# Performance work log

Hardware: AMD Instinct MI355X
Metric: run time of the kernel (lower is better)

## Reference

```python
import jax, jax.numpy as jnp
import numpy as np

C_IN = 64      # in_channels
C_OUT = 64     # out_channels
LOC = 2        # locality_size
K = 2 * LOC + 1   # kernel size = 5
B, H, W = 4, 128, 128


def _init_lateral_weights():
    # Matches LateralLayer._init_lateral_weights: 1 at (co, co*K*K + LOC*K + LOC)
    w = np.zeros((C_OUT, C_IN * K * K), np.float32)
    for co in range(C_OUT):
        cii = co * K * K + LOC * K + LOC  # center tap of matching input channel
        w[co, cii] = 1.0
    return jnp.asarray(w).reshape(C_OUT, C_IN * K * K, 1, 1)


def setup_inputs() -> dict:
    key = jax.random.key(0)
    # binary input (the layer asserts x in {0,1})
    x = jax.random.bernoulli(key, 0.1, (B, C_IN, H, W)).astype(jnp.float32)
    return {"x": x, "W_lateral": _init_lateral_weights()}


def _rearrange(x):
    # Faithful to F.conv2d(x, W_rearrange, padding='same') with the one-hot
    # indicator kernel: out[b, i*K*K + j*K + kk, h, w] = x_pad[b, i, h+j, w+kk].
    # Implemented as an unfold via K*K shifted slices (same math, no O((CKK)^2) conv).
    p = LOC
    xp = jnp.pad(x, ((0, 0), (0, 0), (p, p), (p, p)))
    Hh, Ww = x.shape[2], x.shape[3]
    patches = [xp[:, :, j:j + Hh, kk:kk + Ww] for j in range(K) for kk in range(K)]
    xr = jnp.stack(patches, axis=2)              # (B, C, K*K, H, W)
    return xr.reshape(x.shape[0], x.shape[1] * K * K, Hh, Ww)


def reference(x, W_lateral):
    xr = _rearrange(x)                                  # (B, C*K*K, H, W)
    w = W_lateral.reshape(W_lateral.shape[0], -1)       # (O, C*K*K)
    # 1x1 conv == channel contraction
    x_lateral = jnp.einsum('bkhw,ok->bohw', xr, w)      # (B, O, H, W)
    # conv with ones_like(W_lateral) == channel sum, same for every out channel
    x_max_act = jnp.sum(xr, axis=1, keepdims=True)      # (B, 1, H, W)
    min_support = float(K)
    x_max_act = jnp.maximum(x_max_act, min_support)
    xn = x_lateral / x_max_act
    xn = xn / (1e-10 + jnp.sum(w, axis=1)[None, :, None, None])
    xn = xn / (1e-10 + jnp.max(xn, axis=(2, 3), keepdims=True))
    # ts == 0 -> no temporal averaging with x_lateral_norm_prev
    x_lateral_bin = (xn ** 3 >= 0.5).astype(jnp.float32)
    return x_lateral, xn, x_lateral_bin
```

## Files before the change

kernel.cpp:

```cpp
#include <hip/hip_runtime.h>

constexpr int Bb  = 4;
constexpr int C   = 64;
constexpr int H   = 128;
constexpr int Wd  = 128;
constexpr int K   = 5;
constexpr int LOC = 2;
constexpr int KK  = K * K;
constexpr int CKK = C * KK;
constexpr int HW  = H * Wd;
constexpr int N   = Bb * C * HW;

typedef float v4f __attribute__((ext_vector_type(4)));

__device__ __forceinline__ float frcp(float x) { return __builtin_amdgcn_rcpf(x); }
__device__ __forceinline__ void nt_store4(float* p, v4f v) {
    __builtin_nontemporal_store(v, reinterpret_cast<v4f*>(p));
}

__global__ void __launch_bounds__(256) k_prep(const float* __restrict__ x,
                                              float* __restrict__ M) {
    __shared__ float S[6][Wd];
    const int t = threadIdx.x;
    const int b = blockIdx.x >> 6;
    const int strip = blockIdx.x & 63;
    const int r0 = strip * 2;

    if (t < 192) {
        const int lr = t >> 5;
        const int c0 = (t & 31) * 4;
        const int gr = r0 - 2 + lr;
        v4f s = {0.f, 0.f, 0.f, 0.f};
        if ((unsigned)gr < (unsigned)H) {
            const float* p = x + (((size_t)b * C) * H + gr) * Wd + c0;
#pragma unroll
            for (int c = 0; c < C; ++c)
                s += *reinterpret_cast<const v4f*>(p + (size_t)c * HW);
        }
        *reinterpret_cast<v4f*>(&S[lr][c0]) = s;
    }
    __syncthreads();

    const int lr = t >> 7;
    const int w  = t & 127;
    const int gr = r0 + lr;
    float s = 0.f;
#pragma unroll
    for (int j = 0; j < K; ++j) {
        const float* row = S[lr + j];
#pragma unroll
        for (int kk = 0; kk < K; ++kk) {
            const int ww = w + kk - LOC;
            if ((unsigned)ww < (unsigned)Wd) s += row[ww];
        }
    }
    M[b * HW + gr * Wd + w] = fmaxf(s, (float)K);
}

__global__ void __launch_bounds__(1024) k_main(
    const float* __restrict__ x, const float* __restrict__ wgt,
    const float* __restrict__ M, float* __restrict__ out0,
    float* __restrict__ out1, float* __restrict__ out2) {
    __shared__ int   s_roff[CKK];
    __shared__ int   s_dj[CKK];
    __shared__ int   s_dk[CKK];
    __shared__ float s_v[CKK];
    __shared__ int   s_cnt;
    __shared__ float s_wsum;
    __shared__ float s_red[16];
    __shared__ float s_rinv;

    const int tid = threadIdx.x;
    const int plane = blockIdx.x;
    const int o = plane & (C - 1);
    const int b = plane >> 6;

    if (tid == 0) { s_cnt = 0; s_wsum = 0.0f; }
    __syncthreads();

    const float* wrow = wgt + o * CKK;
    for (int k = tid; k < CKK; k += 1024) {
        float v = wrow[k];
        if (v != 0.0f) {
            int pos = atomicAdd(&s_cnt, 1);
            const int c  = k / KK;
            const int r  = k - c * KK;
            const int rj = r / K;
            const int dj = rj - LOC;
            const int dk = (r - rj * K) - LOC;
            s_roff[pos] = c * HW + dj * Wd;
            s_dj[pos]   = dj;
            s_dk[pos]   = dk;
            s_v[pos]    = v;
            atomicAdd(&s_wsum, v);
        }
    }
    __syncthreads();
    const int   n   = s_cnt;
    const float rws = frcp(1e-10f + s_wsum);

    const float* xb = x + (size_t)b * C * HW;
    float* o0 = out0 + (size_t)plane * HW;
    float* o1 = out1 + (size_t)plane * HW;
    float* o2 = out2 + (size_t)plane * HW;
    const float* Mb = M + b * HW;

    v4f t[4];
    float lmax = -INFINITY;
#pragma unroll
    for (int it = 0; it < 4; ++it) {
        const int p = it * 4096 + tid * 4;
        const int h = p >> 7, w = p & 127;
        v4f acc = {0.f, 0.f, 0.f, 0.f};
        for (int e = 0; e < n; ++e) {
            const float v  = s_v[e];
            const int   hh = h + s_dj[e];
            if ((unsigned)hh < (unsigned)H) {
                const float* rowp = xb + s_roff[e] + h * Wd;
                const int wb = w + s_dk[e];
                float x0 = ((unsigned)(wb + 0) < (unsigned)Wd) ? rowp[wb + 0] : 0.f;
                float x1 = ((unsigned)(wb + 1) < (unsigned)Wd) ? rowp[wb + 1] : 0.f;
                float x2 = ((unsigned)(wb + 2) < (unsigned)Wd) ? rowp[wb + 2] : 0.f;
                float x3 = ((unsigned)(wb + 3) < (unsigned)Wd) ? rowp[wb + 3] : 0.f;
                acc.x += v * x0; acc.y += v * x1; acc.z += v * x2; acc.w += v * x3;
            }
        }
        nt_store4(o0 + p, acc);
        const v4f Mv = *reinterpret_cast<const v4f*>(Mb + p);
        v4f tv;
        tv.x = acc.x * frcp(Mv.x) * rws;
        tv.y = acc.y * frcp(Mv.y) * rws;
        tv.z = acc.z * frcp(Mv.z) * rws;
        tv.w = acc.w * frcp(Mv.w) * rws;
        t[it] = tv;
        lmax = fmaxf(lmax, fmaxf(fmaxf(tv.x, tv.y), fmaxf(tv.z, tv.w)));
    }

#pragma unroll
    for (int m = 32; m > 0; m >>= 1) lmax = fmaxf(lmax, __shfl_xor(lmax, m, 64));
    if ((tid & 63) == 0) s_red[tid >> 6] = lmax;
    __syncthreads();
    if (tid == 0) {
        float r = s_red[0];
#pragma unroll
        for (int q = 1; q < 16; ++q) r = fmaxf(r, s_red[q]);
        s_rinv = frcp(1e-10f + r);
    }
    __syncthreads();
    const float rinv = s_rinv;

#pragma unroll
    for (int it = 0; it < 4; ++it) {
        const int p = it * 4096 + tid * 4;
        const v4f tv = t[it];
        v4f xn, bn;
        xn = tv * rinv;
        bn.x = (xn.x * xn.x * xn.x >= 0.5f) ? 1.f : 0.f;
        bn.y = (xn.y * xn.y * xn.y >= 0.5f) ? 1.f : 0.f;
        bn.z = (xn.z * xn.z * xn.z >= 0.5f) ? 1.f : 0.f;
        bn.w = (xn.w * xn.w * xn.w >= 0.5f) ? 1.f : 0.f;
        nt_store4(o1 + p, xn);
        nt_store4(o2 + p, bn);
    }
}

extern "C" void kernel_launch(void* const* d_in, const int* in_sizes, int n_in,
                              void* d_out, int out_size, void* d_ws, size_t ws_size,
                              hipStream_t stream) {
    const float* x   = (const float*)d_in[0];
    const float* wgt = (const float*)d_in[1];
    float* out = (float*)d_out;
    float* M   = (float*)d_ws;

    float* out0 = out;
    float* out1 = out + N;
    float* out2 = out + 2 * N;

    k_prep<<<Bb * 64, 256, 0, stream>>>(x, M);
    k_main<<<Bb * C, 1024, 0, stream>>>(x, wgt, M, out0, out1, out2);
}
```

Before: 91.63 us.

## Split prep channel sum across threads, precompute reciprocal, add aligned-tap fast path

The prep kernel now uses 768 threads that each sum a 16-channel chunk, reduces the partial sums through shared memory, and stores the reciprocal of the clamped support count instead of the count. The main kernel loads these reciprocals into registers before the weight scan, packs tap metadata into a single int4 in shared memory, and takes a vectorised float4 load path when the horizontal tap offset is zero. The aim is more memory parallelism in prep, less per-element rcp work, and fewer scalar loads in the hot tap loop. In exchange it uses more shared memory in prep and adds a branch in the inner loop.

Measured after the change: 91.79 us. About the same (+0.2%).

```diff
diff --git a/kernel.cpp b/kernel.cpp
--- a/kernel.cpp
+++ b/kernel.cpp
@@ -18,53 +18,66 @@
     __builtin_nontemporal_store(v, reinterpret_cast<v4f*>(p));
 }
 
-__global__ void __launch_bounds__(256) k_prep(const float* __restrict__ x,
-                                              float* __restrict__ M) {
+__global__ void __launch_bounds__(768) k_prep(const float* __restrict__ x,
+                                              float* __restrict__ RM) {
+    __shared__ float P[4][6][Wd];
     __shared__ float S[6][Wd];
     const int t = threadIdx.x;
     const int b = blockIdx.x >> 6;
     const int strip = blockIdx.x & 63;
     const int r0 = strip * 2;
 
+    {
+        const int chunk = t / 192;
+        const int slot  = t - chunk * 192;
+        const int lr = slot >> 5;
+        const int c0 = (slot & 31) * 4;
+        const int gr = r0 - 2 + lr;
+        v4f s = {0.f, 0.f, 0.f, 0.f};
+        if ((unsigned)gr < (unsigned)H) {
+            const float* p = x + (((size_t)b * C + chunk * 16) * H + gr) * Wd + c0;
+#pragma unroll
+            for (int c = 0; c < 16; ++c)
+                s += *reinterpret_cast<const v4f*>(p + (size_t)c * HW);
+        }
+        *reinterpret_cast<v4f*>(&P[chunk][lr][c0]) = s;
+    }
+    __syncthreads();
+
     if (t < 192) {
         const int lr = t >> 5;
         const int c0 = (t & 31) * 4;
-        const int gr = r0 - 2 + lr;
-        v4f s = {0.f, 0.f, 0.f, 0.f};
-        if ((unsigned)gr < (unsigned)H) {
-            const float* p = x + (((size_t)b * C) * H + gr) * Wd + c0;
-#pragma unroll
-            for (int c = 0; c < C; ++c)
-                s += *reinterpret_cast<const v4f*>(p + (size_t)c * HW);
-        }
+        v4f s = *reinterpret_cast<v4f*>(&P[0][lr][c0])
+              + *reinterpret_cast<v4f*>(&P[1][lr][c0])
+              + *reinterpret_cast<v4f*>(&P[2][lr][c0])
+              + *reinterpret_cast<v4f*>(&P[3][lr][c0]);
         *reinterpret_cast<v4f*>(&S[lr][c0]) = s;
     }
     __syncthreads();
 
-    const int lr = t >> 7;
-    const int w  = t & 127;
-    const int gr = r0 + lr;
-    float s = 0.f;
-#pragma unroll
-    for (int j = 0; j < K; ++j) {
-        const float* row = S[lr + j];
-#pragma unroll
-        for (int kk = 0; kk < K; ++kk) {
-            const int ww = w + kk - LOC;
-            if ((unsigned)ww < (unsigned)Wd) s += row[ww];
-        }
-    }
-    M[b * HW + gr * Wd + w] = fmaxf(s, (float)K);
+    if (t < 256) {
+        const int lr = t >> 7;
+        const int w  = t & 127;
+        const int gr = r0 + lr;
+        float s = 0.f;
+#pragma unroll
+        for (int j = 0; j < K; ++j) {
+            const float* row = S[lr + j];
+#pragma unroll
+            for (int kk = 0; kk < K; ++kk) {
+                const int ww = w + kk - LOC;
+                if ((unsigned)ww < (unsigned)Wd) s += row[ww];
+            }
+        }
+        RM[b * HW + gr * Wd + w] = frcp(fmaxf(s, (float)K));
+    }
 }
 
 __global__ void __launch_bounds__(1024) k_main(
     const float* __restrict__ x, const float* __restrict__ wgt,
-    const float* __restrict__ M, float* __restrict__ out0,
+    const float* __restrict__ RM, float* __restrict__ out0,
     float* __restrict__ out1, float* __restrict__ out2) {
-    __shared__ int   s_roff[CKK];
-    __shared__ int   s_dj[CKK];
-    __shared__ int   s_dk[CKK];
-    __shared__ float s_v[CKK];
+    __shared__ int4  s_tap[CKK];
     __shared__ int   s_cnt;
     __shared__ float s_wsum;
     __shared__ float s_red[16];
@@ -74,6 +87,14 @@
     const int plane = blockIdx.x;
     const int o = plane & (C - 1);
     const int b = plane >> 6;
+
+    const float* xb  = x + (size_t)b * C * HW;
+    const float* RMb = RM + b * HW;
+
+    v4f rm[4];
+#pragma unroll
+    for (int it = 0; it < 4; ++it)
+        rm[it] = *reinterpret_cast<const v4f*>(RMb + it * 4096 + tid * 4);
 
     if (tid == 0) { s_cnt = 0; s_wsum = 0.0f; }
     __syncthreads();
@@ -88,10 +109,12 @@
             const int rj = r / K;
             const int dj = rj - LOC;
             const int dk = (r - rj * K) - LOC;
-            s_roff[pos] = c * HW + dj * Wd;
-            s_dj[pos]   = dj;
-            s_dk[pos]   = dk;
-            s_v[pos]    = v;
+            int4 tp;
+            tp.x = c * HW + dj * Wd;
+            tp.y = dj;
+            tp.z = dk;
+            tp.w = __float_as_int(v);
+            s_tap[pos] = tp;
             atomicAdd(&s_wsum, v);
         }
     }
@@ -99,13 +122,11 @@
     const int   n   = s_cnt;
     const float rws = frcp(1e-10f + s_wsum);
 
-    const float* xb = x + (size_t)b * C * HW;
     float* o0 = out0 + (size_t)plane * HW;
     float* o1 = out1 + (size_t)plane * HW;
     float* o2 = out2 + (size_t)plane * HW;
-    const float* Mb = M + b * HW;
-
-    v4f t[4];
+
+    v4f tt[4];
     float lmax = -INFINITY;
 #pragma unroll
     for (int it = 0; it < 4; ++it) {
@@ -113,26 +134,32 @@
         const int h = p >> 7, w = p & 127;
         v4f acc = {0.f, 0.f, 0.f, 0.f};
         for (int e = 0; e < n; ++e) {
-            const float v  = s_v[e];
-            const int   hh = h + s_dj[e];
+            const int4 tp = s_tap[e];
+            const float v = __int_as_float(tp.w);
+            const int hh = h + tp.y;
             if ((unsigned)hh < (unsigned)H) {
-                const float* rowp = xb + s_roff[e] + h * Wd;
-                const int wb = w + s_dk[e];
-                float x0 = ((unsigned)(wb + 0) < (unsigned)Wd) ? rowp[wb + 0] : 0.f;
-                float x1 = ((unsigned)(wb + 1) < (unsigned)Wd) ? rowp[wb + 1] : 0.f;
-                float x2 = ((unsigned)(wb + 2) < (unsigned)Wd) ? rowp[wb + 2] : 0.f;
-                float x3 = ((unsigned)(wb + 3) < (unsigned)Wd) ? rowp[wb + 3] : 0.f;
-                acc.x += v * x0; acc.y += v * x1; acc.z += v * x2; acc.w += v * x3;
+                if (tp.z == 0) {
+                    const v4f xv = *reinterpret_cast<const v4f*>(xb + tp.x + p);
+                    acc.x += v * xv.x; acc.y += v * xv.y;
+                    acc.z += v * xv.z; acc.w += v * xv.w;
+                } else {
+                    const float* rowp = xb + tp.x + h * Wd;
+                    const int wb = w + tp.z;
+                    float x0 = ((unsigned)(wb + 0) < (unsigned)Wd) ? rowp[wb + 0] : 0.f;
+                    float x1 = ((unsigned)(wb + 1) < (unsigned)Wd) ? rowp[wb + 1] : 0.f;
+                    float x2 = ((unsigned)(wb + 2) < (unsigned)Wd) ? rowp[wb + 2] : 0.f;
+                    float x3 = ((unsigned)(wb + 3) < (unsigned)Wd) ? rowp[wb + 3] : 0.f;
+                    acc.x += v * x0; acc.y += v * x1; acc.z += v * x2; acc.w += v * x3;
+                }
             }
         }
         nt_store4(o0 + p, acc);
-        const v4f Mv = *reinterpret_cast<const v4f*>(Mb + p);
         v4f tv;
-        tv.x = acc.x * frcp(Mv.x) * rws;
-        tv.y = acc.y * frcp(Mv.y) * rws;
-        tv.z = acc.z * frcp(Mv.z) * rws;
-        tv.w = acc.w * frcp(Mv.w) * rws;
-        t[it] = tv;
+        tv.x = acc.x * rm[it].x * rws;
+        tv.y = acc.y * rm[it].y * rws;
+        tv.z = acc.z * rm[it].z * rws;
+        tv.w = acc.w * rm[it].w * rws;
+        tt[it] = tv;
         lmax = fmaxf(lmax, fmaxf(fmaxf(tv.x, tv.y), fmaxf(tv.z, tv.w)));
     }
 
@@ -152,7 +179,7 @@
 #pragma unroll
     for (int it = 0; it < 4; ++it) {
         const int p = it * 4096 + tid * 4;
-        const v4f tv = t[it];
+        const v4f tv = tt[it];
         v4f xn, bn;
         xn = tv * rinv;
         bn.x = (xn.x * xn.x * xn.x >= 0.5f) ? 1.f : 0.f;
@@ -170,12 +197,12 @@
     const float* x   = (const float*)d_in[0];
     const float* wgt = (const float*)d_in[1];
     float* out = (float*)d_out;
-    float* M   = (float*)d_ws;
+    float* RMw = (float*)d_ws;
 
     float* out0 = out;
     float* out1 = out + N;
     float* out2 = out + 2 * N;
 
-    k_prep<<<Bb * 64, 256, 0, stream>>>(x, M);
-    k_main<<<Bb * C, 1024, 0, stream>>>(x, wgt, M, out0, out1, out2);
-}
+    k_prep<<<Bb * 64, 768, 0, stream>>>(x, RMw);
+    k_main<<<Bb * C, 1024, 0, stream>>>(x, wgt, RMw, out0, out1, out2);
+}
```
